# Kernel tuning notes

Hardware: AMD Instinct MI355X
Metric: run time of the kernel (lower is better)

## Reference

```python
import jax, jax.numpy as jnp
import numpy as np

V, T, D, L, H, F = 32000, 1024, 768, 8, 12, 3072
DH = D // H
SCALE = 1.0 / np.sqrt(DH)
EPS = 1e-5


def layer_norm(x, w, b):
    mu = jnp.mean(x, axis=-1, keepdims=True)
    var = jnp.mean(jnp.square(x - mu), axis=-1, keepdims=True)
    return (x - mu) * jax.lax.rsqrt(var + EPS) * w + b


def setup_inputs() -> dict:
    key = jax.random.key(0)
    ks = jax.random.split(key, 10)
    def nrm(k, shape, std=0.02):
        return (jax.random.normal(k, shape, dtype=jnp.float32) * std)
    inp = {
        "idx": jax.random.randint(ks[0], (4, T), 0, V, dtype=jnp.int32),
        "targets": jax.random.randint(ks[1], (4, T), 0, V, dtype=jnp.int32),
        "tok_emb": nrm(ks[2], (V, D)),
        "pos_emb": nrm(ks[3], (T, D)),
        "qkv_w": nrm(ks[4], (L, 3 * D, D)),
        "qkv_b": jnp.zeros((L, 3 * D), jnp.float32),
        "proj_w": nrm(ks[5], (L, D, D)),
        "proj_b": jnp.zeros((L, D), jnp.float32),
        "fc1_w": nrm(ks[6], (L, F, D)),
        "fc1_b": jnp.zeros((L, F), jnp.float32),
        "fc2_w": nrm(ks[7], (L, D, F)),
        "fc2_b": jnp.zeros((L, D), jnp.float32),
        "ln1_w": jnp.ones((L, D), jnp.float32),
        "ln1_b": jnp.zeros((L, D), jnp.float32),
        "ln2_w": jnp.ones((L, D), jnp.float32),
        "ln2_b": jnp.zeros((L, D), jnp.float32),
        "lnf_w": jnp.ones((D,), jnp.float32),
        "lnf_b": jnp.zeros((D,), jnp.float32),
    }
    return inp


def gpt_forward(idx, targets, tok_emb, pos_emb, qkv_w, qkv_b, proj_w, proj_b,
                fc1_w, fc1_b, fc2_w, fc2_b, ln1_w, ln1_b, ln2_w, ln2_b, lnf_w, lnf_b):
    B, Tc = idx.shape
    x = tok_emb[idx] + pos_emb[:Tc][None]  # [B,T,D]
    causal = jnp.tril(jnp.ones((Tc, Tc), bool))

    def block(x, p):
        qw, qb, pw, pb, f1w, f1b, f2w, f2b, l1w, l1b, l2w, l2b = p
        h = layer_norm(x, l1w, l1b)
        qkv = h @ qw.T + qb  # [B,T,3D]
        q, k, v = jnp.split(qkv, 3, axis=-1)
        q = q.reshape(B, Tc, H, DH).transpose(0, 2, 1, 3)  # [B,H,T,DH]
        k = k.reshape(B, Tc, H, DH).transpose(0, 2, 1, 3)
        v = v.reshape(B, Tc, H, DH).transpose(0, 2, 1, 3)
        att = jnp.einsum('bhqd,bhkd->bhqk', q, k) * SCALE
        att = jnp.where(causal, att, -jnp.inf)
        att = jax.nn.softmax(att, axis=-1)
        y = jnp.einsum('bhqk,bhkd->bhqd', att, v)
        y = y.transpose(0, 2, 1, 3).reshape(B, Tc, D)
        x = x + y @ pw.T + pb
        h2 = layer_norm(x, l2w, l2b)
        x = x + jax.nn.gelu(h2 @ f1w.T + f1b, approximate=False) @ f2w.T + f2b
        return x, None

    x, _ = jax.lax.scan(block, x, (qkv_w, qkv_b, proj_w, proj_b,
                                   fc1_w, fc1_b, fc2_w, fc2_b,
                                   ln1_w, ln1_b, ln2_w, ln2_b))
    x = layer_norm(x, lnf_w, lnf_b)
    logits = jnp.einsum('btd,vd->btv', x, tok_emb)  # tied lm_head, output_mult=1
    logp = jax.nn.log_softmax(logits, axis=-1)
    valid = targets != -100
    tgt = jnp.where(valid, targets, 0)
    nll = -jnp.take_along_axis(logp, tgt[..., None], axis=-1)[..., 0]
    loss = jnp.sum(nll * valid) / jnp.maximum(jnp.sum(valid), 1)
    return logits, loss


def reference(idx, targets, tok_emb, pos_emb, qkv_w, qkv_b, proj_w, proj_b,
              fc1_w, fc1_b, fc2_w, fc2_b, ln1_w, ln1_b, ln2_w, ln2_b, lnf_w, lnf_b):
    return gpt_forward(idx, targets, tok_emb, pos_emb, qkv_w, qkv_b, proj_w, proj_b,
                       fc1_w, fc1_b, fc2_w, fc2_b, ln1_w, ln1_b, ln2_w, ln2_b, lnf_w, lnf_b)
```

## Files before the change

### kernel.cpp

```cpp
#include <hip/hip_runtime.h>
#include <hip/hip_bf16.h>
#include <math.h>

#define BATCH 4
#define T 1024
#define D 768
#define L 8
#define H 12
#define F 3072
#define V 32000
#define DH 64
#define M (BATCH*T)
#define D3 (3*D)
#define SCALE 0.125f
#define VCHUNK 6400
#define PBT 125

typedef unsigned short u16;
typedef __attribute__((ext_vector_type(8))) short bf16x8;
typedef __attribute__((ext_vector_type(4))) float f32x4;

__device__ inline u16 f2b(float f) {
  __hip_bfloat16 h = __float2bfloat16(f);
  return *(u16*)&h;
}

__device__ inline void gll16(const void* g, void* l) {
  __builtin_amdgcn_global_load_lds(
      (const __attribute__((address_space(1))) unsigned int*)g,
      (__attribute__((address_space(3))) unsigned int*)l, 16, 0, 0);
}

__device__ inline int swzi(int r, int c) {
  return (r * 64 + c) ^ ((((r & 7) ^ ((r >> 3) & 7))) << 3);
}

__device__ inline float block_reduce(float v, bool is_max, float* buf4) {
  int lane = threadIdx.x & 63, wid = threadIdx.x >> 6;
#pragma unroll
  for (int off = 32; off; off >>= 1) {
    float o = __shfl_down(v, off, 64);
    v = is_max ? fmaxf(v, o) : v + o;
  }
  if (lane == 0) buf4[wid] = v;
  __syncthreads();
  float r = is_max ? fmaxf(fmaxf(buf4[0], buf4[1]), fmaxf(buf4[2], buf4[3]))
                   : buf4[0] + buf4[1] + buf4[2] + buf4[3];
  __syncthreads();
  return r;
}

__global__ __launch_bounds__(256) void k_embed(const int* __restrict__ idx,
                                               const float* __restrict__ tok,
                                               const float* __restrict__ pos,
                                               float* __restrict__ x) {
  int i = blockIdx.x * 256 + threadIdx.x;
  int row = i / D, d = i - row * D;
  int t = row & (T - 1);
  x[i] = tok[(size_t)idx[row] * D + d] + pos[(size_t)t * D + d];
}

__global__ __launch_bounds__(256) void k_cvt(const float* __restrict__ in,
                                             u16* __restrict__ out, int n4) {
  int i = blockIdx.x * 256 + threadIdx.x;
  if (i >= n4) return;
  float4 v = ((const float4*)in)[i];
  ushort4 o;
  o.x = f2b(v.x); o.y = f2b(v.y); o.z = f2b(v.z); o.w = f2b(v.w);
  ((ushort4*)out)[i] = o;
}

__global__ __launch_bounds__(256) void k_cvtw(const float* __restrict__ q,
                                              const float* __restrict__ p,
                                              const float* __restrict__ f1,
                                              const float* __restrict__ f2,
                                              u16* __restrict__ out) {
  const int N0 = L * D3 * D / 4, N1 = L * D * D / 4;
  const int N2 = L * F * D / 4, N3 = L * D * F / 4;
  int i = blockIdx.x * 256 + threadIdx.x;
  if (i >= N0 + N1 + N2 + N3) return;
  const float* src;
  int j = i;
  if (i < N0) { src = q; }
  else if (i < N0 + N1) { src = p; j = i - N0; }
  else if (i < N0 + N1 + N2) { src = f1; j = i - N0 - N1; }
  else { src = f2; j = i - N0 - N1 - N2; }
  float4 v = ((const float4*)src)[j];
  ushort4 o;
  o.x = f2b(v.x); o.y = f2b(v.y); o.z = f2b(v.z); o.w = f2b(v.w);
  ((ushort4*)out)[i] = o;
}

__global__ __launch_bounds__(256) void k_lnorm(const float* __restrict__ x,
                                               const float* __restrict__ w,
                                               const float* __restrict__ b,
                                               u16* __restrict__ out) {
  int lane = threadIdx.x & 63, wid = threadIdx.x >> 6;
  int row = blockIdx.x * 4 + wid;
  const float4* xr = (const float4*)(x + (size_t)row * D);
  float4 v[3];
  float s = 0.f, ss = 0.f;
#pragma unroll
  for (int p = 0; p < 3; ++p) {
    v[p] = xr[lane + 64 * p];
    s += v[p].x + v[p].y + v[p].z + v[p].w;
    ss += v[p].x * v[p].x + v[p].y * v[p].y + v[p].z * v[p].z + v[p].w * v[p].w;
  }
#pragma unroll
  for (int off = 32; off; off >>= 1) {
    s += __shfl_xor(s, off, 64);
    ss += __shfl_xor(ss, off, 64);
  }
  float mu = s * (1.0f / D);
  float var = ss * (1.0f / D) - mu * mu;
  float rs = rsqrtf(var + 1e-5f);
  ushort4* orow = (ushort4*)(out + (size_t)row * D);
#pragma unroll
  for (int p = 0; p < 3; ++p) {
    float4 wv = ((const float4*)w)[lane + 64 * p];
    float4 bv = ((const float4*)b)[lane + 64 * p];
    ushort4 o;
    o.x = f2b((v[p].x - mu) * rs * wv.x + bv.x);
    o.y = f2b((v[p].y - mu) * rs * wv.y + bv.y);
    o.z = f2b((v[p].z - mu) * rs * wv.z + bv.z);
    o.w = f2b((v[p].w - mu) * rs * wv.w + bv.w);
    orow[lane + 64 * p] = o;
  }
}

__global__ __launch_bounds__(512, 2) void k_gemm8(
    const u16* __restrict__ A, const u16* __restrict__ W,
    const float* __restrict__ bias, const float* __restrict__ resid,
    void* __restrict__ Cout, int K, int ldC, int flags) {
  __shared__ __attribute__((aligned(16))) u16 lds[2][2][128 * 64];
  int tid = threadIdx.x, w = tid >> 6, lane = tid & 63;
  int wm = w >> 2, wn = w & 3;
  int bn = blockIdx.x, bm = blockIdx.y;
  int frow = lane & 15, g = lane >> 4;
  int sr = lane >> 3, scu = lane & 7;
  const u16* Ab = A + (size_t)bm * 128 * K;
  const u16* Wb = W + (size_t)bn * 128 * K;
  int NT = K >> 6;

  f32x4 acc[4][2];
#pragma unroll
  for (int i = 0; i < 4; ++i)
#pragma unroll
    for (int j = 0; j < 2; ++j) acc[i][j] = (f32x4)(0.f);

#define STG(t)                                                            \
  {                                                                       \
    _Pragma("unroll") for (int rr = 0; rr < 2; ++rr) {                    \
      int row = rr * 64 + w * 8 + sr;                                     \
      int gcu = scu ^ (row & 7);                                          \
      gll16(Ab + (size_t)row * K + (t) * 64 + gcu * 8,                    \
            &lds[(t) & 1][0][(rr * 64 + w * 8) * 64]);                    \
      gll16(Wb + (size_t)row * K + (t) * 64 + gcu * 8,                    \
            &lds[(t) & 1][1][(rr * 64 + w * 8) * 64]);                    \
    }                                                                     \
  }

  STG(0);
  asm volatile("s_waitcnt vmcnt(0)");
  __builtin_amdgcn_s_barrier();

  for (int t = 0; t < NT; ++t) {
    if (t + 1 < NT) {
      STG(t + 1);
      asm volatile("s_waitcnt vmcnt(4)");
    } else {
      asm volatile("s_waitcnt vmcnt(0)");
    }
    __builtin_amdgcn_s_barrier();
    const u16* bA = &lds[t & 1][0][0];
    const u16* bB = &lds[t & 1][1][0];
    bf16x8 ar[8], br[4];
#pragma unroll
    for (int i = 0; i < 4; ++i)
#pragma unroll
      for (int kk = 0; kk < 2; ++kk) {
        int r = wm * 64 + i * 16 + frow;
        ar[i * 2 + kk] = *(const bf16x8*)(bA + r * 64 + ((g + kk * 4) ^ (r & 7)) * 8);
      }
#pragma unroll
    for (int j = 0; j < 2; ++j)
#pragma unroll
      for (int kk = 0; kk < 2; ++kk) {
        int r = wn * 32 + j * 16 + frow;
        br[j * 2 + kk] = *(const bf16x8*)(bB + r * 64 + ((g + kk * 4) ^ (r & 7)) * 8);
      }
    __builtin_amdgcn_s_setprio(1);
#pragma unroll
    for (int i = 0; i < 4; ++i)
#pragma unroll
      for (int j = 0; j < 2; ++j)
#pragma unroll
        for (int kk = 0; kk < 2; ++kk)
          acc[i][j] = __builtin_amdgcn_mfma_f32_16x16x32_bf16(
              ar[i * 2 + kk], br[j * 2 + kk], acc[i][j], 0, 0, 0);
    __builtin_amdgcn_s_setprio(0);
    __builtin_amdgcn_s_barrier();
  }
#undef STG

  int m0 = bm * 128 + wm * 64 + g * 4;
  int n0 = bn * 128 + wn * 32 + frow;
#pragma unroll
  for (int i = 0; i < 4; ++i) {
#pragma unroll
    for (int j = 0; j < 2; ++j) {
      int n = n0 + j * 16;
      float bv = (flags & 1) ? bias[n] : 0.f;
#pragma unroll
      for (int q = 0; q < 4; ++q) {
        int m = m0 + i * 16 + q;
        size_t off = (size_t)m * ldC + n;
        float v = acc[i][j][q] + bv;
        if (flags & 4) v = 0.5f * v * (1.0f + erff(v * 0.70710678118f));
        if (flags & 2) v += resid[off];
        if (flags & 8) ((u16*)Cout)[off] = f2b(v);
        else           ((float*)Cout)[off] = v;
      }
    }
  }
}

__global__ __launch_bounds__(512, 2) void k_lm256(
    const u16* __restrict__ A,
    const u16* __restrict__ B,
    float* __restrict__ C,
    float* __restrict__ pm, float* __restrict__ ps,
    int gc0) {
  __shared__ __attribute__((aligned(16))) u16 lds[2][2][2][128 * 64];
  __shared__ float pml[256][4], psl[256][4];
  const int K = 768, NT = 12;
  int tid = threadIdx.x, w = tid >> 6, lane = tid & 63;
  int wm = w >> 2, wn = w & 3;
  int bm = blockIdx.y, bn = blockIdx.x;
  int frow = lane & 15, g = lane >> 4;
  int sr = lane >> 3, scu = lane & 7;
  const u16* Abase = A + (size_t)bm * 256 * K;
  const u16* Bbase = B + (size_t)bn * 256 * K;

  f32x4 acc[8][4];
#pragma unroll
  for (int i = 0; i < 8; ++i)
#pragma unroll
    for (int j = 0; j < 4; ++j) acc[i][j] = (f32x4)(0.f);

#define STAGE(t, h)                                                       \
  {                                                                       \
    const u16* src = ((h) < 2 ? Abase : Bbase) + (size_t)(((h)&1) * 128) * K; \
    u16* dst = &lds[(t) & 1][(h) >> 1][(h)&1][0];                         \
    _Pragma("unroll") for (int rr = 0; rr < 2; ++rr) {                    \
      int row = rr * 64 + w * 8 + sr;                                     \
      int gcu = scu ^ (row & 7);                                          \
      gll16(src + (size_t)row * K + (t) * 64 + gcu * 8,                   \
            dst + (rr * 64 + w * 8) * 64);                                \
    }                                                                     \
  }

  bf16x8 ar[8], br[8];
#define LDA(T_, ILO)                                                      \
  {                                                                       \
    const u16* base = &lds[(T_)&1][0][wm][0];                             \
    _Pragma("unroll") for (int ii = 0; ii < 4; ++ii)                      \
    _Pragma("unroll") for (int kk = 0; kk < 2; ++kk) {                    \
      int ri = ((ILO) + ii) * 16 + frow;                                  \
      int u = (g + kk * 4) ^ (ri & 7);                                    \
      ar[ii * 2 + kk] = *(const bf16x8*)(base + ri * 64 + u * 8);         \
    }                                                                     \
  }
#define LDB(T_, JLO, BO)                                                  \
  {                                                                       \
    const u16* base = &lds[(T_)&1][1][wn >> 1][0];                        \
    _Pragma("unroll") for (int jj = 0; jj < 2; ++jj)                      \
    _Pragma("unroll") for (int kk = 0; kk < 2; ++kk) {                    \
      int rj = (wn & 1) * 64 + ((JLO) + jj) * 16 + frow;                  \
      int u = (g + kk * 4) ^ (rj & 7);                                    \
      br[(BO) + jj * 2 + kk] = *(const bf16x8*)(base + rj * 64 + u * 8);  \
    }                                                                     \
  }
#define MFMA16(ILO, JLO, BO)                                              \
  _Pragma("unroll") for (int ii = 0; ii < 4; ++ii)                        \
  _Pragma("unroll") for (int jj = 0; jj < 2; ++jj)                        \
  _Pragma("unroll") for (int kk = 0; kk < 2; ++kk)                        \
    acc[(ILO) + ii][(JLO) + jj] = __builtin_amdgcn_mfma_f32_16x16x32_bf16( \
        ar[ii * 2 + kk], br[(BO) + jj * 2 + kk], acc[(ILO) + ii][(JLO) + jj], 0, 0, 0);

  STAGE(0, 0); STAGE(0, 1); STAGE(0, 2); STAGE(0, 3);
  asm volatile("s_waitcnt vmcnt(0)");
  __builtin_amdgcn_s_barrier();

  for (int t = 0; t < NT; ++t) {
    bool pf = (t + 1 < NT);
    LDA(t, 0); LDB(t, 0, 0);
    if (pf) { STAGE(t + 1, 0); STAGE(t + 1, 1); }
    __builtin_amdgcn_s_setprio(1);
    MFMA16(0, 0, 0);
    __builtin_amdgcn_s_setprio(0);
    __builtin_amdgcn_s_barrier();
    LDB(t, 2, 4);
    if (pf) { STAGE(t + 1, 2); STAGE(t + 1, 3); }
    __builtin_amdgcn_s_setprio(1);
    MFMA16(0, 2, 4);
    __builtin_amdgcn_s_setprio(0);
    __builtin_amdgcn_s_barrier();
    LDA(t, 4);
    __builtin_amdgcn_s_setprio(1);
    MFMA16(4, 2, 4);
    __builtin_amdgcn_s_setprio(0);
    __builtin_amdgcn_s_barrier();
    __builtin_amdgcn_s_setprio(1);
    MFMA16(4, 0, 0);
    __builtin_amdgcn_s_setprio(0);
    asm volatile("s_waitcnt vmcnt(0)");
    __builtin_amdgcn_s_barrier();
  }

#pragma unroll
  for (int ii = 0; ii < 8; ++ii) {
#pragma unroll
    for (int q = 0; q < 4; ++q) {
      float mx = fmaxf(fmaxf(acc[ii][0][q], acc[ii][1][q]),
                       fmaxf(acc[ii][2][q], acc[ii][3][q]));
      mx = fmaxf(mx, __shfl_xor(mx, 1, 64));
      mx = fmaxf(mx, __shfl_xor(mx, 2, 64));
      mx = fmaxf(mx, __shfl_xor(mx, 4, 64));
      mx = fmaxf(mx, __shfl_xor(mx, 8, 64));
      float sm = 0.f;
#pragma unroll
      for (int jj = 0; jj < 4; ++jj) sm += __expf(acc[ii][jj][q] - mx);
      sm += __shfl_xor(sm, 1, 64);
      sm += __shfl_xor(sm, 2, 64);
      sm += __shfl_xor(sm, 4, 64);
      sm += __shfl_xor(sm, 8, 64);
      int lrow = wm * 128 + ii * 16 + g * 4 + q;
      if (frow == 0) { pml[lrow][wn] = mx; psl[lrow][wn] = sm; }
      size_t off = (size_t)(bm * 256 + lrow) * V + gc0 + bn * 256 + wn * 64 + frow;
#pragma unroll
      for (int jj = 0; jj < 4; ++jj) C[off + jj * 16] = acc[ii][jj][q];
    }
  }
  __syncthreads();
  if (tid < 256) {
    float m = fmaxf(fmaxf(pml[tid][0], pml[tid][1]), fmaxf(pml[tid][2], pml[tid][3]));
    float s = 0.f;
#pragma unroll
    for (int w4 = 0; w4 < 4; ++w4) s += psl[tid][w4] * __expf(pml[tid][w4] - m);
    size_t grow = bm * 256 + tid;
    int pb = gc0 / 256 + bn;
    pm[grow * PBT + pb] = m;
    ps[grow * PBT + pb] = s;
  }
#undef STAGE
#undef LDA
#undef LDB
#undef MFMA16
}

__global__ __launch_bounds__(256) void k_fattn(const u16* __restrict__ qkv,
                                               u16* __restrict__ y) {
  __shared__ __attribute__((aligned(16))) u16 lQ[2][64 * 64];
  __shared__ __attribute__((aligned(16))) u16 lK[64 * 64];
  __shared__ __attribute__((aligned(16))) u16 lVt[64 * 64];
  __shared__ __attribute__((aligned(16))) u16 lP[64 * 64];
  int tid = threadIdx.x;
  int w = tid >> 6, lane = tid & 63;
  int xi = blockIdx.x;
  int bh = blockIdx.y, b = bh / H, h = bh - b * H;
  int qt[2];
  qt[0] = 15 - xi;
  qt[1] = xi;
  const u16* base = qkv + (size_t)b * T * D3 + h * DH;
  int srow = lane >> 3;
  int scu = lane & 7;
  int frow = lane & 15, g = lane >> 4;
  int w16 = w * 16;
  int qrow = g * 4;

#pragma unroll
  for (int tq = 0; tq < 2; ++tq)
#pragma unroll
    for (int c = 0; c < 2; ++c) {
      int row = c * 32 + w * 8 + srow;
      int gcu = scu ^ (row & 7);
      gll16(base + (size_t)(qt[tq] * 64 + row) * D3 + gcu * 8,
            &lQ[tq][(c * 32 + w * 8) * 64]);
    }

  float m_r[2][4], l_r[2][4];
  f32x4 o[2][4];
#pragma unroll
  for (int s = 0; s < 2; ++s)
#pragma unroll
    for (int i = 0; i < 4; ++i) {
      m_r[s][i] = -1e30f; l_r[s][i] = 0.f; o[s][i] = (f32x4)(0.f);
    }

  int ktmax = 15 - xi;
  uint4 kr[2], vr[2];
#pragma unroll
  for (int c = 0; c < 2; ++c) {
    int row = c * 32 + w * 8 + srow;
    kr[c] = *(const uint4*)(base + D + (size_t)row * D3 + scu * 8);
    vr[c] = *(const uint4*)(base + 2 * D + (size_t)row * D3 + scu * 8);
  }

  for (int kt = 0; kt <= ktmax; ++kt) {
    __syncthreads();
    int k0 = kt * 64;
#pragma unroll
    for (int c = 0; c < 2; ++c) {
      int row = c * 32 + w * 8 + srow;
      *(uint4*)(lK + row * 64 + (scu ^ (row & 7)) * 8) = kr[c];
      unsigned vals[4] = {vr[c].x, vr[c].y, vr[c].z, vr[c].w};
#pragma unroll
      for (int e = 0; e < 4; ++e) {
        lVt[swzi(scu * 8 + 2 * e, row)]     = (u16)(vals[e] & 0xffff);
        lVt[swzi(scu * 8 + 2 * e + 1, row)] = (u16)(vals[e] >> 16);
      }
    }
    __syncthreads();
    if (kt < ktmax) {
      int k0n = k0 + 64;
#pragma unroll
      for (int c = 0; c < 2; ++c) {
        int row = c * 32 + w * 8 + srow;
        kr[c] = *(const uint4*)(base + D + (size_t)(k0n + row) * D3 + scu * 8);
        vr[c] = *(const uint4*)(base + 2 * D + (size_t)(k0n + row) * D3 + scu * 8);
      }
    }

#pragma unroll
    for (int tq = 0; tq < 2; ++tq) {
      if (tq == 1 && kt > xi) continue;
      bool diag = (kt == qt[tq]);
      int qglob0 = qt[tq] * 64 + w16;
      int f7 = frow & 7;
      const u16* lq = &lQ[tq][0];
      bf16x8 aq0 = *(const bf16x8*)(lq + (w16 + frow) * 64 + (g ^ f7) * 8);
      bf16x8 aq1 = *(const bf16x8*)(lq + (w16 + frow) * 64 + ((g + 4) ^ f7) * 8);
      f32x4 sv[4];
#pragma unroll
      for (int kn = 0; kn < 4; ++kn) {
        bf16x8 bk0 = *(const bf16x8*)(lK + (kn * 16 + frow) * 64 + (g ^ f7) * 8);
        bf16x8 bk1 = *(const bf16x8*)(lK + (kn * 16 + frow) * 64 + ((g + 4) ^ f7) * 8);
        sv[kn] = __builtin_amdgcn_mfma_f32_16x16x32_bf16(aq0, bk0, (f32x4)(0.f), 0, 0, 0);
        sv[kn] = __builtin_amdgcn_mfma_f32_16x16x32_bf16(aq1, bk1, sv[kn], 0, 0, 0);
      }
#pragma unroll
      for (int kn = 0; kn < 4; ++kn)
#pragma unroll
        for (int qi = 0; qi < 4; ++qi) {
          float v = sv[kn][qi] * SCALE;
          if (diag) {
            int qg = qglob0 + qrow + qi;
            int kg = k0 + kn * 16 + frow;
            if (kg > qg) v = -1e30f;
          }
          sv[kn][qi] = v;
        }
#pragma unroll
      for (int qi = 0; qi < 4; ++qi) {
        float rm = fmaxf(fmaxf(sv[0][qi], sv[1][qi]), fmaxf(sv[2][qi], sv[3][qi]));
        rm = fmaxf(rm, __shfl_xor(rm, 1, 64));
        rm = fmaxf(rm, __shfl_xor(rm, 2, 64));
        rm = fmaxf(rm, __shfl_xor(rm, 4, 64));
        rm = fmaxf(rm, __shfl_xor(rm, 8, 64));
        float mn = fmaxf(m_r[tq][qi], rm);
        float alpha = __expf(m_r[tq][qi] - mn);
        m_r[tq][qi] = mn;
        float rs = 0.f;
#pragma unroll
        for (int kn = 0; kn < 4; ++kn) {
          float p = __expf(sv[kn][qi] - mn);
          sv[kn][qi] = p;
          rs += p;
        }
        rs += __shfl_xor(rs, 1, 64);
        rs += __shfl_xor(rs, 2, 64);
        rs += __shfl_xor(rs, 4, 64);
        rs += __shfl_xor(rs, 8, 64);
        l_r[tq][qi] = l_r[tq][qi] * alpha + rs;
#pragma unroll
        for (int df = 0; df < 4; ++df) o[tq][df][qi] *= alpha;
      }
#pragma unroll
      for (int kn = 0; kn < 4; ++kn)
#pragma unroll
        for (int qi = 0; qi < 4; ++qi)
          lP[swzi(w16 + qrow + qi, kn * 16 + frow)] = f2b(sv[kn][qi]);
      bf16x8 pa0 = *(const bf16x8*)(lP + swzi(w16 + frow, g * 8));
      bf16x8 pa1 = *(const bf16x8*)(lP + swzi(w16 + frow, 32 + g * 8));
#pragma unroll
      for (int df = 0; df < 4; ++df) {
        bf16x8 bv0 = *(const bf16x8*)(lVt + swzi(df * 16 + frow, g * 8));
        bf16x8 bv1 = *(const bf16x8*)(lVt + swzi(df * 16 + frow, 32 + g * 8));
        o[tq][df] = __builtin_amdgcn_mfma_f32_16x16x32_bf16(pa0, bv0, o[tq][df], 0, 0, 0);
        o[tq][df] = __builtin_amdgcn_mfma_f32_16x16x32_bf16(pa1, bv1, o[tq][df], 0, 0, 0);
      }
    }
  }

#pragma unroll
  for (int tq = 0; tq < 2; ++tq)
#pragma unroll
    for (int df = 0; df < 4; ++df)
#pragma unroll
      for (int qi = 0; qi < 4; ++qi) {
        int qg = qt[tq] * 64 + w16 + qrow + qi;
        y[(size_t)(b * T + qg) * D + h * DH + df * 16 + frow] =
            f2b(o[tq][df][qi] / l_r[tq][qi]);
      }
}

__global__ __launch_bounds__(256) void k_loss_rows(
    const float* __restrict__ pm, const float* __restrict__ ps,
    const float* __restrict__ logits, const int* __restrict__ targets,
    float* __restrict__ nll) {
  int lane = threadIdx.x & 63, wid = threadIdx.x >> 6;
  int row = blockIdx.x * 4 + wid;
  const float* pmr = pm + (size_t)row * PBT;
  const float* psr = ps + (size_t)row * PBT;
  float m = -1e30f;
  for (int i = lane; i < PBT; i += 64) m = fmaxf(m, pmr[i]);
#pragma unroll
  for (int off = 32; off; off >>= 1) m = fmaxf(m, __shfl_xor(m, off, 64));
  float s = 0.f;
  for (int i = lane; i < PBT; i += 64) s += psr[i] * __expf(pmr[i] - m);
#pragma unroll
  for (int off = 32; off; off >>= 1) s += __shfl_xor(s, off, 64);
  if (lane == 0) {
    int tgt = targets[row];
    nll[row] = (tgt != -100) ? (m + logf(s) - logits[(size_t)row * V + tgt]) : 0.f;
  }
}

__global__ __launch_bounds__(256) void k_loss_final(const float* __restrict__ nll,
                                                    const int* __restrict__ targets,
                                                    float* __restrict__ out) {
  __shared__ float buf4[4];
  float s = 0.f, c = 0.f;
  for (int i = threadIdx.x; i < M; i += 256) {
    s += nll[i];
    c += (targets[i] != -100) ? 1.f : 0.f;
  }
  s = block_reduce(s, false, buf4);
  c = block_reduce(c, false, buf4);
  if (threadIdx.x == 0) out[0] = s / fmaxf(c, 1.f);
}

extern "C" void kernel_launch(void* const* d_in, const int* in_sizes, int n_in,
                              void* d_out, int out_size, void* d_ws, size_t ws_size,
                              hipStream_t stream) {
  const int* idx       = (const int*)d_in[0];
  const int* targets   = (const int*)d_in[1];
  const float* tok     = (const float*)d_in[2];
  const float* pos     = (const float*)d_in[3];
  const float* qkv_w   = (const float*)d_in[4];
  const float* qkv_b   = (const float*)d_in[5];
  const float* proj_w  = (const float*)d_in[6];
  const float* proj_b  = (const float*)d_in[7];
  const float* fc1_w   = (const float*)d_in[8];
  const float* fc1_b   = (const float*)d_in[9];
  const float* fc2_w   = (const float*)d_in[10];
  const float* fc2_b   = (const float*)d_in[11];
  const float* ln1_w   = (const float*)d_in[12];
  const float* ln1_b   = (const float*)d_in[13];
  const float* ln2_w   = (const float*)d_in[14];
  const float* ln2_b   = (const float*)d_in[15];
  const float* lnf_w   = (const float*)d_in[16];
  const float* lnf_b   = (const float*)d_in[17];

  float* logits = (float*)d_out;

  char* ws = (char*)d_ws;
  float* x   = (float*)ws;
  u16* hb    = (u16*)(ws + 12582912);
  u16* yb    = (u16*)(ws + 18874368);
  u16* wb    = (u16*)(ws + 25165824);
  float* pm  = (float*)(ws + 34996224);
  float* ps  = (float*)(ws + 37044224);
  float* nll = (float*)(ws + 39092224);

  u16* qkvb   = (u16*)logits;
  u16* f1b    = (u16*)(logits + 9437184);
  u16* wqkv   = (u16*)(logits + 15728640);
  u16* wproj  = (u16*)(logits + 22806528);
  u16* wfc1   = (u16*)(logits + 25165824);
  u16* wfc2   = (u16*)(logits + 34603008);

  {
    const int NW4 = (L * D3 * D + L * D * D + L * F * D + L * D * F) / 4;
    k_cvtw<<<(NW4 + 255) / 256, 256, 0, stream>>>(qkv_w, proj_w, fc1_w, fc2_w, wqkv);
  }

  k_embed<<<(M * D) / 256, 256, 0, stream>>>(idx, tok, pos, x);

  for (int l = 0; l < L; ++l) {
    k_lnorm<<<M / 4, 256, 0, stream>>>(x, ln1_w + (size_t)l * D, ln1_b + (size_t)l * D, hb);
    k_gemm8<<<dim3(D3 / 128, M / 128), 512, 0, stream>>>(
        hb, wqkv + (size_t)l * D3 * D, qkv_b + (size_t)l * D3, nullptr, qkvb, D, D3, 9);
    k_fattn<<<dim3(8, BATCH * H), 256, 0, stream>>>(qkvb, yb);
    k_gemm8<<<dim3(D / 128, M / 128), 512, 0, stream>>>(
        yb, wproj + (size_t)l * D * D, proj_b + (size_t)l * D, x, x, D, D, 3);
    k_lnorm<<<M / 4, 256, 0, stream>>>(x, ln2_w + (size_t)l * D, ln2_b + (size_t)l * D, hb);
    k_gemm8<<<dim3(F / 128, M / 128), 512, 0, stream>>>(
        hb, wfc1 + (size_t)l * F * D, fc1_b + (size_t)l * F, nullptr, f1b, D, F, 13);
    k_gemm8<<<dim3(D / 128, M / 128), 512, 0, stream>>>(
        f1b, wfc2 + (size_t)l * D * F, fc2_b + (size_t)l * D, x, x, F, D, 3);
  }

  k_lnorm<<<M / 4, 256, 0, stream>>>(x, lnf_w, lnf_b, hb);
  for (int c = 0; c < 5; ++c) {
    k_cvt<<<(VCHUNK * D / 4 + 255) / 256, 256, 0, stream>>>(
        tok + (size_t)c * VCHUNK * D, wb, VCHUNK * D / 4);
    k_lm256<<<dim3(VCHUNK / 256, M / 256), 512, 0, stream>>>(
        hb, wb, logits, pm, ps, c * VCHUNK);
  }
  k_loss_rows<<<M / 4, 256, 0, stream>>>(pm, ps, logits, targets, nll);
  k_loss_final<<<1, 256, 0, stream>>>(nll, targets, logits + (size_t)M * V);
}
```

Measured before the change: 1.999 ms.

## Split attention query tiles across 8 waves and run LM head in one pass

The flash-attention kernel moves from 256 to 512 threads, so each of the two paired query tiles gets its own four waves instead of one wave set handling both tiles in turn. This shortens each wave's serial work and raises parallelism, in exchange for a larger P buffer in shared memory and more threads per block. When the workspace is large enough, the tied-embedding conversion and LM-head GEMM run once over the full vocabulary rather than in five chunks, which cuts launch count and improves GPU fill. If the workspace is too small, the chunked path is kept.

```diff
diff --git a/kernel.cpp b/kernel.cpp
--- a/kernel.cpp
+++ b/kernel.cpp
@@ -359,88 +359,68 @@
 #undef MFMA16
 }
 
-__global__ __launch_bounds__(256) void k_fattn(const u16* __restrict__ qkv,
+__global__ __launch_bounds__(512) void k_fattn(const u16* __restrict__ qkv,
                                                u16* __restrict__ y) {
   __shared__ __attribute__((aligned(16))) u16 lQ[2][64 * 64];
   __shared__ __attribute__((aligned(16))) u16 lK[64 * 64];
   __shared__ __attribute__((aligned(16))) u16 lVt[64 * 64];
-  __shared__ __attribute__((aligned(16))) u16 lP[64 * 64];
+  __shared__ __attribute__((aligned(16))) u16 lP[128 * 64];
   int tid = threadIdx.x;
   int w = tid >> 6, lane = tid & 63;
+  int tq = w >> 2, ws4 = w & 3;
   int xi = blockIdx.x;
   int bh = blockIdx.y, b = bh / H, h = bh - b * H;
-  int qt[2];
-  qt[0] = 15 - xi;
-  qt[1] = xi;
+  int myqt = tq ? xi : (15 - xi);
   const u16* base = qkv + (size_t)b * T * D3 + h * DH;
   int srow = lane >> 3;
   int scu = lane & 7;
   int frow = lane & 15, g = lane >> 4;
-  int w16 = w * 16;
+  int s16 = ws4 * 16;
   int qrow = g * 4;
-
-#pragma unroll
-  for (int tq = 0; tq < 2; ++tq)
-#pragma unroll
-    for (int c = 0; c < 2; ++c) {
-      int row = c * 32 + w * 8 + srow;
-      int gcu = scu ^ (row & 7);
-      gll16(base + (size_t)(qt[tq] * 64 + row) * D3 + gcu * 8,
-            &lQ[tq][(c * 32 + w * 8) * 64]);
-    }
-
-  float m_r[2][4], l_r[2][4];
-  f32x4 o[2][4];
-#pragma unroll
-  for (int s = 0; s < 2; ++s)
-#pragma unroll
-    for (int i = 0; i < 4; ++i) {
-      m_r[s][i] = -1e30f; l_r[s][i] = 0.f; o[s][i] = (f32x4)(0.f);
-    }
+  int f7 = frow & 7;
+
+#pragma unroll
+  for (int c = 0; c < 2; ++c) {
+    int row = s16 + c * 8 + srow;
+    int gcu = scu ^ (row & 7);
+    gll16(base + (size_t)(myqt * 64 + row) * D3 + gcu * 8,
+          &lQ[tq][(s16 + c * 8) * 64]);
+  }
+
+  float m_r[4], l_r[4];
+  f32x4 o[4];
+#pragma unroll
+  for (int i = 0; i < 4; ++i) { m_r[i] = -1e30f; l_r[i] = 0.f; o[i] = (f32x4)(0.f); }
 
   int ktmax = 15 - xi;
-  uint4 kr[2], vr[2];
-#pragma unroll
-  for (int c = 0; c < 2; ++c) {
-    int row = c * 32 + w * 8 + srow;
-    kr[c] = *(const uint4*)(base + D + (size_t)row * D3 + scu * 8);
-    vr[c] = *(const uint4*)(base + 2 * D + (size_t)row * D3 + scu * 8);
-  }
+  int kvrow = w * 8 + srow;
+  uint4 kr = *(const uint4*)(base + D + (size_t)kvrow * D3 + scu * 8);
+  uint4 vr = *(const uint4*)(base + 2 * D + (size_t)kvrow * D3 + scu * 8);
 
   for (int kt = 0; kt <= ktmax; ++kt) {
     __syncthreads();
     int k0 = kt * 64;
-#pragma unroll
-    for (int c = 0; c < 2; ++c) {
-      int row = c * 32 + w * 8 + srow;
-      *(uint4*)(lK + row * 64 + (scu ^ (row & 7)) * 8) = kr[c];
-      unsigned vals[4] = {vr[c].x, vr[c].y, vr[c].z, vr[c].w};
+    *(uint4*)(lK + kvrow * 64 + (scu ^ (kvrow & 7)) * 8) = kr;
+    {
+      unsigned vals[4] = {vr.x, vr.y, vr.z, vr.w};
 #pragma unroll
       for (int e = 0; e < 4; ++e) {
-        lVt[swzi(scu * 8 + 2 * e, row)]     = (u16)(vals[e] & 0xffff);
-        lVt[swzi(scu * 8 + 2 * e + 1, row)] = (u16)(vals[e] >> 16);
+        lVt[swzi(scu * 8 + 2 * e, kvrow)]     = (u16)(vals[e] & 0xffff);
+        lVt[swzi(scu * 8 + 2 * e + 1, kvrow)] = (u16)(vals[e] >> 16);
       }
     }
     __syncthreads();
     if (kt < ktmax) {
-      int k0n = k0 + 64;
-#pragma unroll
-      for (int c = 0; c < 2; ++c) {
-        int row = c * 32 + w * 8 + srow;
-        kr[c] = *(const uint4*)(base + D + (size_t)(k0n + row) * D3 + scu * 8);
-        vr[c] = *(const uint4*)(base + 2 * D + (size_t)(k0n + row) * D3 + scu * 8);
-      }
-    }
-
-#pragma unroll
-    for (int tq = 0; tq < 2; ++tq) {
-      if (tq == 1 && kt > xi) continue;
-      bool diag = (kt == qt[tq]);
-      int qglob0 = qt[tq] * 64 + w16;
-      int f7 = frow & 7;
+      int rown = k0 + 64 + kvrow;
+      kr = *(const uint4*)(base + D + (size_t)rown * D3 + scu * 8);
+      vr = *(const uint4*)(base + 2 * D + (size_t)rown * D3 + scu * 8);
+    }
+
+    if (tq == 0 || kt <= xi) {
+      bool diag = (kt == myqt);
       const u16* lq = &lQ[tq][0];
-      bf16x8 aq0 = *(const bf16x8*)(lq + (w16 + frow) * 64 + (g ^ f7) * 8);
-      bf16x8 aq1 = *(const bf16x8*)(lq + (w16 + frow) * 64 + ((g + 4) ^ f7) * 8);
+      bf16x8 aq0 = *(const bf16x8*)(lq + (s16 + frow) * 64 + (g ^ f7) * 8);
+      bf16x8 aq1 = *(const bf16x8*)(lq + (s16 + frow) * 64 + ((g + 4) ^ f7) * 8);
       f32x4 sv[4];
 #pragma unroll
       for (int kn = 0; kn < 4; ++kn) {
@@ -455,7 +435,7 @@
         for (int qi = 0; qi < 4; ++qi) {
           float v = sv[kn][qi] * SCALE;
           if (diag) {
-            int qg = qglob0 + qrow + qi;
+            int qg = myqt * 64 + s16 + qrow + qi;
             int kg = k0 + kn * 16 + frow;
             if (kg > qg) v = -1e30f;
           }
@@ -468,9 +448,9 @@
         rm = fmaxf(rm, __shfl_xor(rm, 2, 64));
         rm = fmaxf(rm, __shfl_xor(rm, 4, 64));
         rm = fmaxf(rm, __shfl_xor(rm, 8, 64));
-        float mn = fmaxf(m_r[tq][qi], rm);
-        float alpha = __expf(m_r[tq][qi] - mn);
-        m_r[tq][qi] = mn;
+        float mn = fmaxf(m_r[qi], rm);
+        float alpha = __expf(m_r[qi] - mn);
+        m_r[qi] = mn;
         float rs = 0.f;
 #pragma unroll
         for (int kn = 0; kn < 4; ++kn) {
@@ -482,37 +462,35 @@
         rs += __shfl_xor(rs, 2, 64);
         rs += __shfl_xor(rs, 4, 64);
         rs += __shfl_xor(rs, 8, 64);
-        l_r[tq][qi] = l_r[tq][qi] * alpha + rs;
-#pragma unroll
-        for (int df = 0; df < 4; ++df) o[tq][df][qi] *= alpha;
+        l_r[qi] = l_r[qi] * alpha + rs;
+#pragma unroll
+        for (int df = 0; df < 4; ++df) o[df][qi] *= alpha;
       }
 #pragma unroll
       for (int kn = 0; kn < 4; ++kn)
 #pragma unroll
         for (int qi = 0; qi < 4; ++qi)
-          lP[swzi(w16 + qrow + qi, kn * 16 + frow)] = f2b(sv[kn][qi]);
-      bf16x8 pa0 = *(const bf16x8*)(lP + swzi(w16 + frow, g * 8));
-      bf16x8 pa1 = *(const bf16x8*)(lP + swzi(w16 + frow, 32 + g * 8));
+          lP[swzi(w * 16 + qrow + qi, kn * 16 + frow)] = f2b(sv[kn][qi]);
+      bf16x8 pa0 = *(const bf16x8*)(lP + swzi(w * 16 + frow, g * 8));
+      bf16x8 pa1 = *(const bf16x8*)(lP + swzi(w * 16 + frow, 32 + g * 8));
 #pragma unroll
       for (int df = 0; df < 4; ++df) {
         bf16x8 bv0 = *(const bf16x8*)(lVt + swzi(df * 16 + frow, g * 8));
         bf16x8 bv1 = *(const bf16x8*)(lVt + swzi(df * 16 + frow, 32 + g * 8));
-        o[tq][df] = __builtin_amdgcn_mfma_f32_16x16x32_bf16(pa0, bv0, o[tq][df], 0, 0, 0);
-        o[tq][df] = __builtin_amdgcn_mfma_f32_16x16x32_bf16(pa1, bv1, o[tq][df], 0, 0, 0);
+        o[df] = __builtin_amdgcn_mfma_f32_16x16x32_bf16(pa0, bv0, o[df], 0, 0, 0);
+        o[df] = __builtin_amdgcn_mfma_f32_16x16x32_bf16(pa1, bv1, o[df], 0, 0, 0);
       }
     }
   }
 
 #pragma unroll
-  for (int tq = 0; tq < 2; ++tq)
-#pragma unroll
-    for (int df = 0; df < 4; ++df)
-#pragma unroll
-      for (int qi = 0; qi < 4; ++qi) {
-        int qg = qt[tq] * 64 + w16 + qrow + qi;
-        y[(size_t)(b * T + qg) * D + h * DH + df * 16 + frow] =
-            f2b(o[tq][df][qi] / l_r[tq][qi]);
-      }
+  for (int df = 0; df < 4; ++df)
+#pragma unroll
+    for (int qi = 0; qi < 4; ++qi) {
+      int qg = myqt * 64 + s16 + qrow + qi;
+      y[(size_t)(b * T + qg) * D + h * DH + df * 16 + frow] =
+          f2b(o[df][qi] / l_r[qi]);
+    }
 }
 
 __global__ __launch_bounds__(256) void k_loss_rows(
@@ -580,9 +558,17 @@
   u16* hb    = (u16*)(ws + 12582912);
   u16* yb    = (u16*)(ws + 18874368);
   u16* wb    = (u16*)(ws + 25165824);
-  float* pm  = (float*)(ws + 34996224);
-  float* ps  = (float*)(ws + 37044224);
-  float* nll = (float*)(ws + 39092224);
+  bool big = ws_size >= (size_t)(25165824 + 49152000 + 2048000 * 2 + 16384);
+  float* pm, * ps, * nll;
+  if (big) {
+    pm  = (float*)(ws + 25165824 + 49152000);
+    ps  = (float*)(ws + 25165824 + 49152000 + 2048000);
+    nll = (float*)(ws + 25165824 + 49152000 + 4096000);
+  } else {
+    pm  = (float*)(ws + 34996224);
+    ps  = (float*)(ws + 37044224);
+    nll = (float*)(ws + 39092224);
+  }
 
   u16* qkvb   = (u16*)logits;
   u16* f1b    = (u16*)(logits + 9437184);
@@ -602,7 +588,7 @@
     k_lnorm<<<M / 4, 256, 0, stream>>>(x, ln1_w + (size_t)l * D, ln1_b + (size_t)l * D, hb);
     k_gemm8<<<dim3(D3 / 128, M / 128), 512, 0, stream>>>(
         hb, wqkv + (size_t)l * D3 * D, qkv_b + (size_t)l * D3, nullptr, qkvb, D, D3, 9);
-    k_fattn<<<dim3(8, BATCH * H), 256, 0, stream>>>(qkvb, yb);
+    k_fattn<<<dim3(8, BATCH * H), 512, 0, stream>>>(qkvb, yb);
     k_gemm8<<<dim3(D / 128, M / 128), 512, 0, stream>>>(
         yb, wproj + (size_t)l * D * D, proj_b + (size_t)l * D, x, x, D, D, 3);
     k_lnorm<<<M / 4, 256, 0, stream>>>(x, ln2_w + (size_t)l * D, ln2_b + (size_t)l * D, hb);
@@ -613,11 +599,17 @@
   }
 
   k_lnorm<<<M / 4, 256, 0, stream>>>(x, lnf_w, lnf_b, hb);
-  for (int c = 0; c < 5; ++c) {
-    k_cvt<<<(VCHUNK * D / 4 + 255) / 256, 256, 0, stream>>>(
-        tok + (size_t)c * VCHUNK * D, wb, VCHUNK * D / 4);
-    k_lm256<<<dim3(VCHUNK / 256, M / 256), 512, 0, stream>>>(
-        hb, wb, logits, pm, ps, c * VCHUNK);
+  if (big) {
+    k_cvt<<<(V * D / 4 + 255) / 256, 256, 0, stream>>>(tok, wb, V * D / 4);
+    k_lm256<<<dim3(V / 256, M / 256), 512, 0, stream>>>(
+        hb, wb, logits, pm, ps, 0);
+  } else {
+    for (int c = 0; c < 5; ++c) {
+      k_cvt<<<(VCHUNK * D / 4 + 255) / 256, 256, 0, stream>>>(
+          tok + (size_t)c * VCHUNK * D, wb, VCHUNK * D / 4);
+      k_lm256<<<dim3(VCHUNK / 256, M / 256), 512, 0, stream>>>(
+          hb, wb, logits, pm, ps, c * VCHUNK);
+    }
   }
   k_loss_rows<<<M / 4, 256, 0, stream>>>(pm, ps, logits, targets, nll);
   k_loss_final<<<1, 256, 0, stream>>>(nll, targets, logits + (size_t)M * V);
```

Result: faster. 1.899 ms (-5.0%).
